# Optimization experiments

Measured on AMD Instinct MI355X. Metric: run time of the kernel, lower is better.

## Reference

```python
import jax, jax.numpy as jnp
import numpy as np
from math import pi

N = 256        # in_features == out_features
BATCH = 131072


def givens_orthogonal(angles, n):
    """Build an n x n orthogonal matrix as the ordered product of Givens
    rotations G(i, j, theta_k) over pairs i < j in lexicographic order.
    Each rotation mixes rows i and j; applied sequentially via lax.scan."""
    ii, jj = np.triu_indices(n, 1)  # static pair order, len = n*(n-1)//2
    ii = jnp.asarray(ii, dtype=jnp.int32)
    jj = jnp.asarray(jj, dtype=jnp.int32)

    def body(M, t):
        i, j, th = t
        c, s = jnp.cos(th), jnp.sin(th)
        ri, rj = M[i], M[j]
        M = M.at[i].set(c * ri - s * rj)
        M = M.at[j].set(s * ri + c * rj)
        return M, None

    M0 = jnp.eye(n, dtype=angles.dtype)
    M, _ = jax.lax.scan(body, M0, (ii, jj, angles))
    return M


def setup_inputs() -> dict:
    key = jax.random.key(0)
    k1, k2, k3 = jax.random.split(key, 3)
    n_ang = N * (N - 1) // 2  # 32640
    return {
        "x": jax.random.normal(k1, (BATCH, N), dtype=jnp.float32),
        "Uweight": jax.random.uniform(k2, (n_ang,), minval=-pi / 2, maxval=pi / 2, dtype=jnp.float32),
        "Vweight": jax.random.uniform(k3, (n_ang,), minval=-pi / 2, maxval=pi / 2, dtype=jnp.float32),
        "Sweight": jnp.ones((N,), dtype=jnp.float32),
        "bias": jnp.zeros((N,), dtype=jnp.float32),
    }


def reference(x, Uweight, Vweight, Sweight, bias):
    # W = V @ diag(S) @ U^T  (SVD-parametrized weight, out x in)
    # y = x @ W^T + b = ((x @ U) * S) @ V^T + b   (square case in == out)
    U = givens_orthogonal(Uweight, N)  # (in, in) orthogonal
    V = givens_orthogonal(Vweight, N)  # (out, out) orthogonal
    return ((x @ U) * Sweight) @ V.T + bias
```

## Files before the change

kernel.cpp:

```cpp
#include <hip/hip_runtime.h>
#include <hip/hip_bf16.h>
#include <math.h>

#define NN 256
#define NSEG 32
#define MAT (NN*NN)

#define MATS0 0
#define MATS1 (MATS0 + 64*MAT)
#define WBT_OFF (MATS1 + 32*MAT)

static __device__ const int BD[NSEG+1] =
    {0,4,8,12,16,20,24,28,32,37,42,47,52,57,62,67,73,79,85,91,97,
     104,111,118,126,134,143,153,164,177,192,213,255};
#define CSL_CAP 1120

typedef __attribute__((ext_vector_type(8))) short short8;
typedef __attribute__((ext_vector_type(4))) float f32x4;

__device__ __forceinline__ short f2bf(float f) {
    __hip_bfloat16 h = __float2bfloat16(f);
    return *reinterpret_cast<short*>(&h);
}

#define BAR() do {                                              \
    asm volatile("s_waitcnt lgkmcnt(0)" ::: "memory");          \
    __builtin_amdgcn_s_barrier();                               \
    asm volatile("" ::: "memory");                              \
} while (0)

__global__ __launch_bounds__(64) void k_build(const float* __restrict__ au,
                                              const float* __restrict__ av,
                                              float* __restrict__ mats) {
    int b = blockIdx.x;
    int matid = b >> 7;
    int seg   = (b >> 2) & 31;
    int chunk = b & 3;
    int t = threadIdx.x;
    int c0 = chunk * 64;
    int i0 = BD[seg], i1 = BD[seg+1];
    float* outp = mats + (matid * NSEG + seg) * MAT;

    if (c0 + 64 <= i0) {
        for (int id = t; id < 4096; id += 64) {
            int row = id >> 4, c4 = (id & 15) * 4;
            float4 v = {0.f,0.f,0.f,0.f};
            int d = row - (c0 + c4);
            if (d >= 0 && d < 4) ((float*)&v)[d] = 1.0f;
            *(float4*)(outp + row*NN + c0 + c4) = v;
        }
        return;
    }

    __shared__ float M[NN * 64];
    __shared__ float2 csl[CSL_CAP];

    int kbase = 255*i0 - (i0*(i0-1))/2;
    int kend  = 255*i1 - (i1*(i1-1))/2;
    int nrot  = kend - kbase;
    const float* ang = (matid ? av : au) + kbase;
    for (int idx = t; idx < nrot; idx += 64) {
        float s, c;
        sincosf(ang[idx], &s, &c);
        float2 v = {c, s};
        csl[idx] = v;
    }

    int MR = NN - i0;
    for (int rr = 0; rr < MR; ++rr)
        M[rr*64 + t] = (i0 + rr == c0 + t) ? 1.0f : 0.0f;
    __syncthreads();

    for (int i = i0; i < i1; ++i) {
        int jstart = (i + 1 > c0) ? (i + 1) : c0;
        int kl = 255*i - (i*(i-1))/2 + (jstart - i - 1) - kbase;
        float ri = M[(i - i0)*64 + t];
        int j = jstart;
        int ng = (NN - jstart) >> 3;

        float2 cb[8]; float rj[8];
        if (ng > 0) {
#pragma unroll
            for (int u = 0; u < 8; ++u) cb[u] = csl[kl + u];
#pragma unroll
            for (int u = 0; u < 8; ++u) rj[u] = M[(j - i0 + u)*64 + t];
        }
        for (int g = 0; g < ng; ++g) {
            float2 cn[8]; float rn[8];
            if (g + 1 < ng) {
#pragma unroll
                for (int u = 0; u < 8; ++u) cn[u] = csl[kl + 8 + u];
#pragma unroll
                for (int u = 0; u < 8; ++u) rn[u] = M[(j + 8 - i0 + u)*64 + t];
            }
#pragma unroll
            for (int u = 0; u < 8; ++u) {
                float wv = cb[u].y*ri + cb[u].x*rj[u];
                ri       = cb[u].x*ri - cb[u].y*rj[u];
                M[(j - i0 + u)*64 + t] = wv;
            }
#pragma unroll
            for (int u = 0; u < 8; ++u) { cb[u] = cn[u]; rj[u] = rn[u]; }
            j += 8; kl += 8;
        }
        int rem = NN - j;
        if (rem > 0) {
            float2 cc[7]; float r7[7];
#pragma unroll
            for (int u = 0; u < 7; ++u)
                if (u < rem) { cc[u] = csl[kl + u];
                               r7[u] = M[(j - i0 + u)*64 + t]; }
#pragma unroll
            for (int u = 0; u < 7; ++u)
                if (u < rem) {
                    float wv = cc[u].y*ri + cc[u].x*r7[u];
                    ri       = cc[u].x*ri - cc[u].y*r7[u];
                    M[(j - i0 + u)*64 + t] = wv;
                }
        }
        M[(i - i0)*64 + t] = ri;
    }
    __syncthreads();

    for (int id = t; id < 4096; id += 64) {
        int row = id >> 4, c4 = (id & 15) * 4;
        float4 v;
        if (row < i0) {
            v = make_float4(0.f,0.f,0.f,0.f);
            int d = row - (c0 + c4);
            if (d >= 0 && d < 4) ((float*)&v)[d] = 1.0f;
        } else {
            v = *(const float4*)&M[(row - i0)*64 + c4];
        }
        *(float4*)(outp + row*NN + c0 + c4) = v;
    }
}

__device__ __forceinline__ void fold_body(const float* __restrict__ in,
                                          float* __restrict__ out,
                                          int nOut, int lg, int span,
                                          int b, int t) {
    int np2 = 2 * nOut;
    int m    = b & (np2 - 1);
    int tile = b >> lg;
    int side = (m >= nOut) ? 1 : 0;
    int q = m - side * nOut;
    const float* A = in + (side*np2 + 2*q + 1) * MAT;
    const float* B = in + (side*np2 + 2*q) * MAT;
    float* C = out + m * MAT;
    int i0A = BD[q * span + (span >> 1)];
    int r0 = (tile >> 2) * 64, c0 = (tile & 3) * 64;

    if (r0 + 64 <= i0A) {
#pragma unroll
        for (int u = 0; u < 4; ++u) {
            int id = u*256 + t;
            int rr = id >> 4, cc = (id & 15) * 4;
            *(float4*)(C + (r0+rr)*NN + c0 + cc) =
                *(const float4*)(B + (r0+rr)*NN + c0 + cc);
        }
        return;
    }

    int kstart = ((r0 < i0A) ? r0 : i0A) & ~31;
    int nt = (NN - kstart) >> 5;

    __shared__ float Ast[2][32][68];
    __shared__ float Bs [2][32][68];
    int tx = t & 15, ty = t >> 4;
    int arow = t >> 3, ak4 = t & 7;
    int bkr = t >> 4, bc4 = t & 15;

    float acc[4][4] = {};
    f32x4 pa0, pa1, pb0, pb1;
    {
        int kt = kstart;
        pa0 = *(const f32x4*)(A + (r0 + arow     )*NN + kt + ak4*4);
        pa1 = *(const f32x4*)(A + (r0 + arow + 32)*NN + kt + ak4*4);
        pb0 = *(const f32x4*)(B + (kt + bkr      )*NN + c0 + bc4*4);
        pb1 = *(const f32x4*)(B + (kt + bkr + 16 )*NN + c0 + bc4*4);
    }
    for (int it = 0; it < nt; ++it) {
        int cur = it & 1;
#pragma unroll
        for (int jj = 0; jj < 4; ++jj) {
            Ast[cur][ak4*4 + jj][arow]      = pa0[jj];
            Ast[cur][ak4*4 + jj][arow + 32] = pa1[jj];
        }
        *(f32x4*)&Bs[cur][bkr     ][bc4*4] = pb0;
        *(f32x4*)&Bs[cur][bkr + 16][bc4*4] = pb1;
        if (it + 1 < nt) {
            int k2 = kstart + (it+1)*32;
            pa0 = *(const f32x4*)(A + (r0 + arow     )*NN + k2 + ak4*4);
            pa1 = *(const f32x4*)(A + (r0 + arow + 32)*NN + k2 + ak4*4);
            pb0 = *(const f32x4*)(B + (k2 + bkr      )*NN + c0 + bc4*4);
            pb1 = *(const f32x4*)(B + (k2 + bkr + 16 )*NN + c0 + bc4*4);
        }
        BAR();
#pragma unroll 8
        for (int kk = 0; kk < 32; ++kk) {
            f32x4 a4 = *(const f32x4*)&Ast[cur][kk][ty*4];
            f32x4 b4 = *(const f32x4*)&Bs [cur][kk][tx*4];
#pragma unroll
            for (int rr = 0; rr < 4; ++rr)
#pragma unroll
                for (int cc = 0; cc < 4; ++cc)
                    acc[rr][cc] = fmaf(a4[rr], b4[cc], acc[rr][cc]);
        }
    }
#pragma unroll
    for (int rr = 0; rr < 4; ++rr) {
        float4 o = {acc[rr][0], acc[rr][1], acc[rr][2], acc[rr][3]};
        *(float4*)(C + (r0 + ty*4 + rr)*NN + c0 + tx*4) = o;
    }
}

__global__ __launch_bounds__(256) void k_fold1(const float* in, float* out)
{ fold_body(in, out, 16, 5,  2, blockIdx.x, threadIdx.x); }
__global__ __launch_bounds__(256) void k_fold2(const float* in, float* out)
{ fold_body(in, out,  8, 4,  4, blockIdx.x, threadIdx.x); }
__global__ __launch_bounds__(256) void k_fold3(const float* in, float* out)
{ fold_body(in, out,  4, 3,  8, blockIdx.x, threadIdx.x); }
__global__ __launch_bounds__(256) void k_fold4(const float* in, float* out)
{ fold_body(in, out,  2, 2, 16, blockIdx.x, threadIdx.x); }
__global__ __launch_bounds__(256) void k_fold5(const float* in, float* out)
{ fold_body(in, out,  1, 1, 32, blockIdx.x, threadIdx.x); }

__global__ __launch_bounds__(256) void k_wmatT(const float* __restrict__ U,
                                               const float* __restrict__ V,
                                               const float* __restrict__ S,
                                               unsigned short* __restrict__ Wbt) {
    int b = blockIdx.x;
    int n0 = (b >> 4) * 16, i0 = (b & 15) * 16;
    int t = threadIdx.x, ti = t & 15, tn = t >> 4;
    __shared__ float Us[16][260];
    __shared__ float Vs[16][260];
    {
        int rr = t >> 4, cc = (t & 15) * 16;
#pragma unroll
        for (int q = 0; q < 4; ++q) {
            float4 u = *(const float4*)(U + (i0+rr)*NN + cc + q*4);
            float4 s = *(const float4*)(S + cc + q*4);
            u.x *= s.x; u.y *= s.y; u.z *= s.z; u.w *= s.w;
            *(float4*)&Us[rr][cc+q*4] = u;
            *(float4*)&Vs[rr][cc+q*4] = *(const float4*)(V + (n0+rr)*NN + cc + q*4);
        }
    }
    __syncthreads();
    float acc = 0.f;
#pragma unroll 8
    for (int k4 = 0; k4 < 64; ++k4) {
        float4 uu = *(const float4*)&Us[ti][k4*4];
        float4 vv = *(const float4*)&Vs[tn][k4*4];
        acc += uu.x*vv.x + uu.y*vv.y + uu.z*vv.z + uu.w*vv.w;
    }
    Wbt[(n0+tn)*NN + (i0+ti)] = (unsigned short)f2bf(acc);
}

__global__ __launch_bounds__(512, 4) void k_mm(const float* __restrict__ x,
                                               const unsigned short* __restrict__ Wbt,
                                               const float* __restrict__ bias,
                                               float* __restrict__ out) {
    int t = threadIdx.x;
    int w = t >> 6, l = t & 63, l15 = l & 15, lg = l >> 4;
    int n0 = w * 32;

    __shared__ unsigned short Xs[2][8 * 512];

    long rowbase = (long)blockIdx.x * 256;
    int r = t & 15, m = t >> 4;
    int ksb = m >> 2;
    int lidx = r + 16 * (m & 3);

    const float* sbase = x + (rowbase + r) * NN + 8*m;
    float4 fa0 = *(const float4*)(sbase);
    float4 fa1 = *(const float4*)(sbase + 4);
    float4 fb0 = *(const float4*)(sbase + 16*NN);
    float4 fb1 = *(const float4*)(sbase + 16*NN + 4);

    short8 bfrag[2][8];
#pragma unroll
    for (int nt = 0; nt < 2; ++nt) {
        const unsigned short* wrow = Wbt + (n0 + nt*16 + l15) * NN + lg * 8;
#pragma unroll
        for (int ks = 0; ks < 8; ++ks)
            bfrag[nt][ks] = *(const short8*)(wrow + ks * 32);
    }
    float b0 = bias[n0 + l15];
    float b1 = bias[n0 + 16 + l15];

#pragma unroll
    for (int it = 0; it < 16; ++it) {
        int cur = it & 1;
        float4 g0 = cur ? fb0 : fa0;
        float4 g1 = cur ? fb1 : fa1;
        short8 h;
        h[0]=f2bf(g0.x); h[1]=f2bf(g0.y); h[2]=f2bf(g0.z); h[3]=f2bf(g0.w);
        h[4]=f2bf(g1.x); h[5]=f2bf(g1.y); h[6]=f2bf(g1.z); h[7]=f2bf(g1.w);
        *(short8*)&Xs[cur][ksb*512 + lidx*8] = h;
        if (it < 14) {
            const float* sn = sbase + (long)(it+2)*16*NN;
            if (cur) { fb0 = *(const float4*)(sn); fb1 = *(const float4*)(sn + 4); }
            else     { fa0 = *(const float4*)(sn); fa1 = *(const float4*)(sn + 4); }
        }
        BAR();

        f32x4 acc0 = {0.f,0.f,0.f,0.f}, acc1 = {0.f,0.f,0.f,0.f};
#pragma unroll
        for (int ks = 0; ks < 8; ++ks) {
            short8 af = *(const short8*)&Xs[cur][ks*512 + l*8];
            acc0 = __builtin_amdgcn_mfma_f32_16x16x32_bf16(af, bfrag[0][ks], acc0, 0, 0, 0);
            acc1 = __builtin_amdgcn_mfma_f32_16x16x32_bf16(af, bfrag[1][ks], acc1, 0, 0, 0);
        }
        float* op = out + (rowbase + it*16 + lg*4) * NN + n0 + l15;
#pragma unroll
        for (int rr = 0; rr < 4; ++rr) {
            op[rr * NN]      = acc0[rr] + b0;
            op[rr * NN + 16] = acc1[rr] + b1;
        }
    }
}

extern "C" void kernel_launch(void* const* d_in, const int* in_sizes, int n_in,
                              void* d_out, int out_size, void* d_ws, size_t ws_size,
                              hipStream_t stream) {
    const float* x    = (const float*)d_in[0];
    const float* Uw   = (const float*)d_in[1];
    const float* Vw   = (const float*)d_in[2];
    const float* Sw   = (const float*)d_in[3];
    const float* bias = (const float*)d_in[4];
    float* out = (float*)d_out;
    float* ws  = (float*)d_ws;

    k_build<<<256, 64, 0, stream>>>(Uw, Vw, ws + MATS0);
    k_fold1<<<16*32, 256, 0, stream>>>(ws + MATS0, ws + MATS1);
    k_fold2<<<16*16, 256, 0, stream>>>(ws + MATS1, ws + MATS0);
    k_fold3<<<16* 8, 256, 0, stream>>>(ws + MATS0, ws + MATS1);
    k_fold4<<<16* 4, 256, 0, stream>>>(ws + MATS1, ws + MATS0);
    k_fold5<<<16* 2, 256, 0, stream>>>(ws + MATS0, ws + MATS1);
    k_wmatT<<<256, 256, 0, stream>>>(ws + MATS1, ws + MATS1 + MAT, Sw,
                                     (unsigned short*)(ws + WBT_OFF));
    k_mm<<<512, 512, 0, stream>>>(x, (unsigned short*)(ws + WBT_OFF), bias, out);
}
```

Measured before the change: 195.1 us.

## Stage full bf16 weight in LDS and give each wave independent row tiles

New measurement: 191.6 us. No clear change (-1.8%).

```diff
diff --git a/kernel.cpp b/kernel.cpp
--- a/kernel.cpp
+++ b/kernel.cpp
@@ -257,66 +257,73 @@
     Wbt[(n0+tn)*NN + (i0+ti)] = (unsigned short)f2bf(acc);
 }
 
-__global__ __launch_bounds__(512, 4) void k_mm(const float* __restrict__ x,
+__global__ __launch_bounds__(512, 1) void k_mm(const float* __restrict__ x,
                                                const unsigned short* __restrict__ Wbt,
                                                const float* __restrict__ bias,
                                                float* __restrict__ out) {
+    __shared__ unsigned short Wl[16 * 8 * 512];
+
     int t = threadIdx.x;
     int w = t >> 6, l = t & 63, l15 = l & 15, lg = l >> 4;
-    int n0 = w * 32;
-
-    __shared__ unsigned short Xs[2][8 * 512];
-
-    long rowbase = (long)blockIdx.x * 256;
-    int r = t & 15, m = t >> 4;
-    int ksb = m >> 2;
-    int lidx = r + 16 * (m & 3);
-
-    const float* sbase = x + (rowbase + r) * NN + 8*m;
-    float4 fa0 = *(const float4*)(sbase);
-    float4 fa1 = *(const float4*)(sbase + 4);
-    float4 fb0 = *(const float4*)(sbase + 16*NN);
-    float4 fb1 = *(const float4*)(sbase + 16*NN + 4);
-
-    short8 bfrag[2][8];
-#pragma unroll
-    for (int nt = 0; nt < 2; ++nt) {
-        const unsigned short* wrow = Wbt + (n0 + nt*16 + l15) * NN + lg * 8;
-#pragma unroll
-        for (int ks = 0; ks < 8; ++ks)
-            bfrag[nt][ks] = *(const short8*)(wrow + ks * 32);
-    }
-    float b0 = bias[n0 + l15];
-    float b1 = bias[n0 + 16 + l15];
-
-#pragma unroll
-    for (int it = 0; it < 16; ++it) {
-        int cur = it & 1;
-        float4 g0 = cur ? fb0 : fa0;
-        float4 g1 = cur ? fb1 : fa1;
-        short8 h;
-        h[0]=f2bf(g0.x); h[1]=f2bf(g0.y); h[2]=f2bf(g0.z); h[3]=f2bf(g0.w);
-        h[4]=f2bf(g1.x); h[5]=f2bf(g1.y); h[6]=f2bf(g1.z); h[7]=f2bf(g1.w);
-        *(short8*)&Xs[cur][ksb*512 + lidx*8] = h;
-        if (it < 14) {
-            const float* sn = sbase + (long)(it+2)*16*NN;
-            if (cur) { fb0 = *(const float4*)(sn); fb1 = *(const float4*)(sn + 4); }
-            else     { fa0 = *(const float4*)(sn); fa1 = *(const float4*)(sn + 4); }
-        }
-        BAR();
-
-        f32x4 acc0 = {0.f,0.f,0.f,0.f}, acc1 = {0.f,0.f,0.f,0.f};
+
+#pragma unroll
+    for (int j = 0; j < 16; ++j) {
+        const unsigned short* src = Wbt + (j*16 + l15)*NN + lg*8 + w*32;
+        *(short8*)&Wl[(j*8 + w)*512 + l*8] = *(const short8*)src;
+    }
+    float bb[16];
+#pragma unroll
+    for (int nt = 0; nt < 16; ++nt) bb[nt] = bias[nt*16 + l15];
+    __syncthreads();
+
+    int gw = blockIdx.x * 8 + w;
+    long rowbase = (long)gw * 64;
+
+    const float* ap = x + (rowbase + l15) * NN + lg*8;
+    float4 ra[8], rb[8];
+#pragma unroll
+    for (int ks = 0; ks < 8; ++ks) {
+        ra[ks] = *(const float4*)(ap + ks*32);
+        rb[ks] = *(const float4*)(ap + ks*32 + 4);
+    }
+
+#pragma unroll
+    for (int it = 0; it < 4; ++it) {
+        short8 af[8];
 #pragma unroll
         for (int ks = 0; ks < 8; ++ks) {
-            short8 af = *(const short8*)&Xs[cur][ks*512 + l*8];
-            acc0 = __builtin_amdgcn_mfma_f32_16x16x32_bf16(af, bfrag[0][ks], acc0, 0, 0, 0);
-            acc1 = __builtin_amdgcn_mfma_f32_16x16x32_bf16(af, bfrag[1][ks], acc1, 0, 0, 0);
-        }
-        float* op = out + (rowbase + it*16 + lg*4) * NN + n0 + l15;
-#pragma unroll
-        for (int rr = 0; rr < 4; ++rr) {
-            op[rr * NN]      = acc0[rr] + b0;
-            op[rr * NN + 16] = acc1[rr] + b1;
+            short8 h;
+            h[0]=f2bf(ra[ks].x); h[1]=f2bf(ra[ks].y);
+            h[2]=f2bf(ra[ks].z); h[3]=f2bf(ra[ks].w);
+            h[4]=f2bf(rb[ks].x); h[5]=f2bf(rb[ks].y);
+            h[6]=f2bf(rb[ks].z); h[7]=f2bf(rb[ks].w);
+            af[ks] = h;
+        }
+        if (it < 3) {
+            const float* np = x + (rowbase + (it+1)*16 + l15) * NN + lg*8;
+#pragma unroll
+            for (int ks = 0; ks < 8; ++ks) {
+                ra[ks] = *(const float4*)(np + ks*32);
+                rb[ks] = *(const float4*)(np + ks*32 + 4);
+            }
+        }
+#pragma unroll
+        for (int p = 0; p < 8; ++p) {
+            int n0t = p*2, n1t = p*2 + 1;
+            f32x4 a0 = {0.f,0.f,0.f,0.f}, a1 = {0.f,0.f,0.f,0.f};
+#pragma unroll
+            for (int ks = 0; ks < 8; ++ks) {
+                short8 b0 = *(const short8*)&Wl[(n0t*8 + ks)*512 + l*8];
+                short8 b1 = *(const short8*)&Wl[(n1t*8 + ks)*512 + l*8];
+                a0 = __builtin_amdgcn_mfma_f32_16x16x32_bf16(af[ks], b0, a0, 0, 0, 0);
+                a1 = __builtin_amdgcn_mfma_f32_16x16x32_bf16(af[ks], b1, a1, 0, 0, 0);
+            }
+            float* op0 = out + (rowbase + it*16 + lg*4) * NN + n0t*16 + l15;
+#pragma unroll
+            for (int rr = 0; rr < 4; ++rr) {
+                op0[rr * NN]      = a0[rr] + bb[n0t];
+                op0[rr * NN + 16] = a1[rr] + bb[n1t];
+            }
         }
     }
 }
@@ -340,5 +347,5 @@
     k_fold5<<<16* 2, 256, 0, stream>>>(ws + MATS0, ws + MATS1);
     k_wmatT<<<256, 256, 0, stream>>>(ws + MATS1, ws + MATS1 + MAT, Sw,
                                      (unsigned short*)(ws + WBT_OFF));
-    k_mm<<<512, 512, 0, stream>>>(x, (unsigned short*)(ws + WBT_OFF), bias, out);
-}
+    k_mm<<<256, 512, 0, stream>>>(x, (unsigned short*)(ws + WBT_OFF), bias, out);
+}
```
